# Kernel tuning notes

Hardware: AMD Instinct MI355X
Metric: run time of the kernel (lower is better)

Reference implementation:

```python
import jax, jax.numpy as jnp
import numpy as np

B, BAG, H, C = 512, 32, 1024, 53
EPS = 1e-8  # torch F.cosine_similarity denominator clamp


def setup_inputs() -> dict:
    key = jax.random.key(0)
    ks = jax.random.split(key, 5)
    return {
        "sent_reps": jax.random.normal(ks[0], (B, BAG, H), jnp.float32),
        "aug_sent_reps": jax.random.normal(ks[1], (B, BAG, H), jnp.float32),
        "rel_table": jax.random.normal(ks[2], (C, H), jnp.float32),
        "cls_w": jax.random.normal(ks[3], (C, H), jnp.float32) * 0.02,
        "cls_b": jnp.zeros((C,), jnp.float32),
        "labels": jax.random.randint(ks[4], (B,), 0, C),
        "temperature": jnp.asarray(0.1, jnp.float32),
    }


def _cl(rep, aug, bag_rep, T):
    # rep, aug: (B, bag, H); bag_rep: (B, H)
    nr = jnp.linalg.norm(rep, axis=-1)        # (B, bag)
    na = jnp.linalg.norm(aug, axis=-1)        # (B, bag)
    nb = jnp.linalg.norm(bag_rep, axis=-1)    # (B,)
    pos_sim = jnp.sum(rep * aug, axis=-1) / jnp.maximum(nr * na, EPS)  # (B, bag)
    pos = jnp.exp(pos_sim / T)
    # pair[c, j, b] = cos(rep[b, j], bag_rep[c])  -- matches torch permute/broadcast chain
    dots = jnp.einsum('bjh,ch->cjb', rep, bag_rep)               # (B, bag, B)
    denom = jnp.maximum(nb[:, None, None] * nr.T[None], EPS)      # (B, bag, B)
    pair = dots / denom
    idx = jnp.arange(rep.shape[0])
    axis_sim = pair[idx, :, idx]                                  # (B, bag): cos(rep[b,j], bag_rep[b])
    neg = jnp.exp(pair / T).sum(axis=2) - jnp.exp(axis_sim / T)   # (B, bag)
    return jnp.mean(-jnp.log(pos / (pos + neg)))


def reference(sent_reps, aug_sent_reps, rel_table, cls_w, cls_b, labels, temperature):
    # Selective attention per bag (scope slices are uniform bags of size BAG -> vectorized)
    rel = rel_table[labels]                                        # (B, H)
    scale = jnp.sqrt(jnp.asarray(H, sent_reps.dtype))
    scores = jnp.einsum('bh,bjh->bj', rel, sent_reps) / scale      # (B, bag)
    alphas = jax.nn.softmax(scores, axis=-1)
    bag_reps = jnp.einsum('bj,bjh->bh', alphas, sent_reps)         # (B, H)
    bag_out = bag_reps @ cls_w.T + cls_b                           # (B, C)  (dropout in eval = identity)
    cl_loss = _cl(sent_reps, aug_sent_reps, bag_reps, temperature)
    return bag_out, cl_loss
```

## Files before the change

### kernel.cpp

```cpp
#include <hip/hip_runtime.h>
#include <hip/hip_bf16.h>


typedef __bf16 bf16x8 __attribute__((ext_vector_type(8)));
typedef __bf16 bf16x4 __attribute__((ext_vector_type(4)));
typedef __bf16 bf16x2 __attribute__((ext_vector_type(2)));
typedef float  f32x4  __attribute__((ext_vector_type(4)));

__device__ inline float wsum(float v) {
    #pragma unroll
    for (int off = 32; off > 0; off >>= 1) v += __shfl_xor(v, off, 64);
    return v;
}

__device__ inline void gll16(const void* g, void* l) {
    __builtin_amdgcn_global_load_lds((const __attribute__((address_space(1))) void*)g,
                                     (__attribute__((address_space(3))) void*)l, 16, 0, 0);
}

__device__ inline f32x4 ntld(const float* p) {
    return __builtin_nontemporal_load((const f32x4*)p);
}

__global__ __launch_bounds__(512, 4) void kab(
    const float* __restrict__ sent, const float* __restrict__ aug,
    const float* __restrict__ rel_table, const int* __restrict__ labels,
    __bf16* __restrict__ repb, float* __restrict__ nr, float* __restrict__ pos_sim,
    const float* __restrict__ clsw, __bf16* __restrict__ cwb,
    __bf16* __restrict__ bagb, float* __restrict__ nbsq, float* __restrict__ loss)
{
    __shared__ __align__(16) __bf16 repS[32][1024];
    __shared__ float scoreS[32], alphaS[32], redS[8];
    const int b = blockIdx.x, t = threadIdx.x;
    const int w = t >> 6, lane = t & 63;

    if (b < 128) {
        const int i = b * 512 + t;
        cwb[i] = (i < 53 * 1024) ? (__bf16)clsw[i] : (__bf16)0.0f;
        if (b == 0 && t == 0) *loss = 0.0f;
    }

    const float* relp = rel_table + (size_t)labels[b] * 1024;
    #pragma unroll
    for (int rr = 0; rr < 4; rr++) {
        const int j = w * 4 + rr;
        const size_t rbase = ((size_t)b * 32 + j) * 1024;
        const float* srow = sent + rbase;
        const float* arow = aug + rbase;
        float P = 0.f, R = 0.f, A = 0.f, D = 0.f;
        #pragma unroll
        for (int i = 0; i < 4; i++) {
            const int h = i * 256 + lane * 4;
            f32x4 v  = ntld(srow + h);
            f32x4 a  = ntld(arow + h);
            f32x4 rl = *(const f32x4*)(relp + h);
            P += v.x * rl.x + v.y * rl.y + v.z * rl.z + v.w * rl.w;
            R += v.x * v.x + v.y * v.y + v.z * v.z + v.w * v.w;
            A += a.x * a.x + a.y * a.y + a.z * a.z + a.w * a.w;
            D += v.x * a.x + v.y * a.y + v.z * a.z + v.w * a.w;
            bf16x4 vb = { (__bf16)v.x, (__bf16)v.y, (__bf16)v.z, (__bf16)v.w };
            *(bf16x4*)(&repS[j][h]) = vb;
            *(bf16x4*)(repb + rbase + h) = vb;
        }
        #pragma unroll
        for (int off = 32; off > 0; off >>= 1) {
            P += __shfl_xor(P, off, 64);
            R += __shfl_xor(R, off, 64);
            A += __shfl_xor(A, off, 64);
            D += __shfl_xor(D, off, 64);
        }
        if (lane == 0) {
            scoreS[j] = P * (1.0f / 32.0f);
            float nrv = sqrtf(R), nav = sqrtf(A);
            nr[b * 32 + j] = nrv;
            pos_sim[b * 32 + j] = D / fmaxf(nrv * nav, 1e-8f);
        }
    }
    __syncthreads();

    if (t < 32) {
        float sj = scoreS[t], mx = sj;
        #pragma unroll
        for (int off = 16; off > 0; off >>= 1) mx = fmaxf(mx, __shfl_xor(mx, off, 32));
        float e = __expf(sj - mx), sm = e;
        #pragma unroll
        for (int off = 16; off > 0; off >>= 1) sm += __shfl_xor(sm, off, 32);
        alphaS[t] = e / sm;
    }
    __syncthreads();

    float b0 = 0.f, b1 = 0.f;
    #pragma unroll 8
    for (int j = 0; j < 32; j++) {
        const float al = alphaS[j];
        bf16x2 v = *(const bf16x2*)(&repS[j][t * 2]);
        b0 += al * (float)v.x;
        b1 += al * (float)v.y;
    }
    bf16x2 bb = { (__bf16)b0, (__bf16)b1 };
    *(bf16x2*)(bagb + (size_t)b * 1024 + t * 2) = bb;

    float q = b0 * b0 + b1 * b1;
    q = wsum(q);
    if (lane == 0) redS[w] = q;
    __syncthreads();
    if (t == 0)
        nbsq[b] = redS[0] + redS[1] + redS[2] + redS[3]
                + redS[4] + redS[5] + redS[6] + redS[7];
}

__global__ __launch_bounds__(512, 2) void k4_gemm(
    const __bf16* __restrict__ repb, const __bf16* __restrict__ bagb,
    const float* __restrict__ nr, const float* __restrict__ nbsq,
    const float* __restrict__ temp, float* __restrict__ partial, float* __restrict__ diag,
    const __bf16* __restrict__ cwb, const float* __restrict__ bias, float* __restrict__ out)
{
    __shared__ __align__(16) char smem[98304];
    const int bid = blockIdx.x;
    const int t = threadIdx.x, lane = t & 63, w = t >> 6;
    const int m = lane & 15, quad = lane >> 4;

    if (bid >= 256) {
        __bf16* Al = (__bf16*)smem;
        __bf16* Bl = (__bf16*)(smem + 8192);
        const int r0 = (bid - 256) * 64;
        f32x4 acc[4] = {};
        const int i0 = (t & 255) * 8;
        const int row0 = i0 >> 5, kk0 = i0 & 31;
        const __bf16* gA = bagb + (size_t)(r0 + row0) * 1024 + kk0;
        const __bf16* gB = cwb + (size_t)row0 * 1024 + kk0;
        const bool act = (t < 256);
        for (int k0 = 0; k0 < 1024; k0 += 64) {
            __syncthreads();
            if (act) {
                gll16(gA + k0,      Al + i0);
                gll16(gA + k0 + 32, Al + 2048 + i0);
                gll16(gB + k0,      Bl + i0);
                gll16(gB + k0 + 32, Bl + 2048 + i0);
            }
            __syncthreads();
            if (act) {
                #pragma unroll
                for (int ks = 0; ks < 2; ks++) {
                    bf16x8 a = *(const bf16x8*)(&Al[ks * 2048 + ((t >> 6) * 16 + m) * 32 + quad * 8]);
                    #pragma unroll
                    for (int n = 0; n < 4; n++) {
                        bf16x8 bf = *(const bf16x8*)(&Bl[ks * 2048 + (n * 16 + m) * 32 + quad * 8]);
                        acc[n] = __builtin_amdgcn_mfma_f32_16x16x32_bf16(a, bf, acc[n], 0, 0, 0);
                    }
                }
            }
        }
        if (act) {
            #pragma unroll
            for (int n = 0; n < 4; n++) {
                const int c = n * 16 + m;
                if (c < 53) {
                    #pragma unroll
                    for (int i = 0; i < 4; i++) {
                        const int r = r0 + (t >> 6) * 16 + quad * 4 + i;
                        out[(size_t)r * 53 + c] = acc[n][i] + bias[c];
                    }
                }
            }
        }
        return;
    }

    float* negp4 = (float*)smem;

    const int xcd = bid & 7, slot = bid >> 3;
    const int cb = slot & 3, rb = (slot >> 2) * 8 + xcd;
    const int r0 = rb * 256, c0 = cb * 128;
    const int wr0 = (w & 3) * 64, wc0 = (w >> 2) * 64;

    const int srow = t >> 2;
    const int scol = 8 * ((t & 3) ^ ((t >> 3) & 3));
    const __bf16* gA0 = repb + (size_t)(r0 + srow) * 1024 + scol;
    const __bf16* gA1 = gA0 + (size_t)128 * 1024;
    const __bf16* gB0 = bagb + (size_t)(c0 + srow) * 1024 + scol;
    const int dA0 = t * 8, dA1 = (t + 512) * 8, dB0 = 8192 + t * 8;

    const int rho = (m >> 1) & 3;
    const int offA = ((wr0 + m) * 4 + (quad ^ rho)) * 8;
    const int offB = 8192 + ((wc0 + m) * 4 + (quad ^ rho)) * 8;

    f32x4 acc[4][4] = {};

    #define BUFB(s) ((__bf16*)(smem + (((s) & 3) * 24576)))
    #define STG(s) do { const int kk_ = (s) * 32; __bf16* b_ = BUFB(s);     \
        gll16(gA0 + kk_, b_ + dA0); gll16(gA1 + kk_, b_ + dA1);             \
        gll16(gB0 + kk_, b_ + dB0); } while (0)

    #define CMP(s) do { const __bf16* b_ = BUFB(s); bf16x8 av_[4], bv_[4];  \
        _Pragma("unroll") for (int i_ = 0; i_ < 4; i_++)                    \
            av_[i_] = *(const bf16x8*)(b_ + offA + i_ * 512);               \
        _Pragma("unroll") for (int n_ = 0; n_ < 4; n_++)                    \
            bv_[n_] = *(const bf16x8*)(b_ + offB + n_ * 512);               \
        _Pragma("unroll") for (int i_ = 0; i_ < 4; i_++)                    \
        _Pragma("unroll") for (int n_ = 0; n_ < 4; n_++)                    \
            acc[i_][n_] = __builtin_amdgcn_mfma_f32_16x16x32_bf16(          \
                av_[i_], bv_[n_], acc[i_][n_], 0, 0, 0); } while (0)

    #define FENCE(N) do { __builtin_amdgcn_sched_barrier(0);                \
        asm volatile("s_waitcnt vmcnt(" #N ")" ::: "memory");               \
        __builtin_amdgcn_s_barrier();                                       \
        __builtin_amdgcn_sched_barrier(0); } while (0)

    STG(0); STG(1); STG(2);
    FENCE(6);
    #pragma unroll 1
    for (int s = 0; s < 29; ++s) {
        STG(s + 3);
        CMP(s);
        FENCE(6);
    }
    CMP(29); FENCE(3);
    CMP(30); FENCE(0);
    CMP(31);

    const float invT = 1.0f / *temp;
    float nrv[16];
    #pragma unroll
    for (int i = 0; i < 4; i++)
        #pragma unroll
        for (int g = 0; g < 4; g++)
            nrv[i * 4 + g] = nr[r0 + wr0 + i * 16 + quad * 4 + g];

    float* myneg = negp4 + (size_t)(w & 3) * 32 * 128;
    #pragma unroll
    for (int n = 0; n < 4; n++) {
        const int c_local = wc0 + n * 16 + m;
        const int cg = c0 + c_local;
        const float nbv = sqrtf(nbsq[cg]);
        #pragma unroll
        for (int i = 0; i < 2; i++) {
            #pragma unroll
            for (int g = 0; g < 4; g++) {
                const int jj = i * 16 + quad * 4 + g;
                const int rg0 = r0 + wr0 + i * 16 + quad * 4 + g;
                const int rg2 = rg0 + 32;
                float e0 = __expf(acc[i][n][g]     / fmaxf(nbv * nrv[i * 4 + g],       1e-8f) * invT);
                float e2 = __expf(acc[i + 2][n][g] / fmaxf(nbv * nrv[(i + 2) * 4 + g], 1e-8f) * invT);
                myneg[jj * 128 + c_local] = e0 + e2;
                if ((rg0 >> 5) == cg) diag[(size_t)cg * 32 + jj] = e0;
                if ((rg2 >> 5) == cg) diag[(size_t)cg * 32 + jj] = e2;
            }
        }
    }
    __syncthreads();

    float* pout = partial + (size_t)rb * 32 * 512 + c0;
    {
        const int jj = t >> 4, c8 = (t & 15) * 8;
        f32x4 v0 = {}, v1 = {};
        #pragma unroll
        for (int p = 0; p < 4; p++) {
            const float* src = negp4 + (size_t)p * 32 * 128 + jj * 128 + c8;
            v0 += *(const f32x4*)(src);
            v1 += *(const f32x4*)(src + 4);
        }
        *(f32x4*)(pout + (size_t)jj * 512 + c8)     = v0;
        *(f32x4*)(pout + (size_t)jj * 512 + c8 + 4) = v1;
    }
    #undef BUFB
    #undef STG
    #undef CMP
    #undef FENCE
}

__global__ __launch_bounds__(256) void k5_neg(
    const float* __restrict__ partial, const float* __restrict__ diag,
    const float* __restrict__ pos_sim, const float* __restrict__ temp,
    float* __restrict__ loss)
{
    const int ct = blockIdx.x & 7, j = blockIdx.x >> 3;
    const int t = threadIdx.x, lane = t & 63, w = t >> 6;
    const int bsub = t >> 4;
    const int cidx = t & 15;
    f32x4 acc = {};
    #pragma unroll
    for (int r = 0; r < 4; r++) {
        const int rb = bsub * 4 + r;
        f32x4 v = *(const f32x4*)(partial + ((size_t)rb * 32 + j) * 512 + ct * 64 + cidx * 4);
        acc += v;
    }
    #pragma unroll
    for (int k = 0; k < 4; k++) {
        acc[k] += __shfl_xor(acc[k], 16, 64);
        acc[k] += __shfl_xor(acc[k], 32, 64);
    }
    __shared__ float red[4][64];
    if (lane < 16) {
        #pragma unroll
        for (int k = 0; k < 4; k++) red[w][lane * 4 + k] = acc[k];
    }
    __syncthreads();

    if (t < 64) {
        const int c = ct * 64 + t;
        float S = red[0][t] + red[1][t] + red[2][t] + red[3][t];
        S -= diag[(size_t)c * 32 + j];
        const float invT = 1.0f / *temp;
        const float lp = pos_sim[(c << 5) + j] * invT;
        float term = logf(__expf(lp) + S) - lp;
        term = wsum(term);
        if (t == 0) atomicAdd(loss, term * (1.0f / 16384.0f));
    }
}

extern "C" void kernel_launch(void* const* d_in, const int* in_sizes, int n_in,
                              void* d_out, int out_size, void* d_ws, size_t ws_size,
                              hipStream_t stream)
{
    const float* sent = (const float*)d_in[0];
    const float* aug  = (const float*)d_in[1];
    const float* rel  = (const float*)d_in[2];
    const float* clsw = (const float*)d_in[3];
    const float* clsb = (const float*)d_in[4];
    const int*   lab  = (const int*)d_in[5];
    const float* temp = (const float*)d_in[6];
    float* out = (float*)d_out;

    char* ws = (char*)d_ws;
    __bf16* bagb    = (__bf16*)(ws);
    float*  nbsq    = (float*)(ws + (1u << 20));
    float*  nr      = (float*)(ws + (1u << 20) + 64 * 1024);
    float*  pos     = (float*)(ws + (1u << 20) + 128 * 1024);
    __bf16* cwb     = (__bf16*)(ws + (1u << 20) + 192 * 1024);
    float*  diag    = (float*)(ws + (2u << 20) + 64 * 1024);
    __bf16* repb    = (__bf16*)(ws + (4u << 20));
    float*  partial = (float*)(ws + (36u << 20));

    float* loss = out + 27136;

    kab    <<<512, 512, 0, stream>>>(sent, aug, rel, lab, repb, nr, pos,
                                     clsw, cwb, bagb, nbsq, loss);
    k4_gemm<<<264, 512, 0, stream>>>(repb, bagb, nr, nbsq, temp, partial, diag,
                                     cwb, clsb, out);
    k5_neg <<<256, 256, 0, stream>>>(partial, diag, pos, temp, loss);
}
```

Baseline: 197.6 us.

## Halve GEMM row tile to 128 with 256-thread blocks and triple-buffered LDS

The contrastive GEMM block shrinks from 256x128 tiles with 8 waves to 128x128 tiles with 4 waves. The grid roughly doubles to 520 blocks, and the LDS pipeline drops from 4 stages to 3 at 48KB. The classifier GEMM blocks move to the front of the grid, and the partial-sum reduction grows to 16 row-blocks. The aim is better occupancy and CU load balance across 256 CUs, in exchange for more partial traffic and less A/B reuse per block.

```diff
diff --git a/kernel.cpp b/kernel.cpp
--- a/kernel.cpp
+++ b/kernel.cpp
@@ -109,88 +109,84 @@
                 + redS[4] + redS[5] + redS[6] + redS[7];
 }
 
-__global__ __launch_bounds__(512, 2) void k4_gemm(
+__global__ __launch_bounds__(256, 3) void k4_gemm(
     const __bf16* __restrict__ repb, const __bf16* __restrict__ bagb,
     const float* __restrict__ nr, const float* __restrict__ nbsq,
     const float* __restrict__ temp, float* __restrict__ partial, float* __restrict__ diag,
     const __bf16* __restrict__ cwb, const float* __restrict__ bias, float* __restrict__ out)
 {
-    __shared__ __align__(16) char smem[98304];
+    __shared__ __align__(16) char smem[49152];
     const int bid = blockIdx.x;
     const int t = threadIdx.x, lane = t & 63, w = t >> 6;
     const int m = lane & 15, quad = lane >> 4;
 
-    if (bid >= 256) {
+    if (bid < 8) {
         __bf16* Al = (__bf16*)smem;
         __bf16* Bl = (__bf16*)(smem + 8192);
-        const int r0 = (bid - 256) * 64;
+        const int r0 = bid * 64;
         f32x4 acc[4] = {};
-        const int i0 = (t & 255) * 8;
+        const int i0 = t * 8;
         const int row0 = i0 >> 5, kk0 = i0 & 31;
         const __bf16* gA = bagb + (size_t)(r0 + row0) * 1024 + kk0;
         const __bf16* gB = cwb + (size_t)row0 * 1024 + kk0;
-        const bool act = (t < 256);
         for (int k0 = 0; k0 < 1024; k0 += 64) {
             __syncthreads();
-            if (act) {
-                gll16(gA + k0,      Al + i0);
-                gll16(gA + k0 + 32, Al + 2048 + i0);
-                gll16(gB + k0,      Bl + i0);
-                gll16(gB + k0 + 32, Bl + 2048 + i0);
-            }
+            gll16(gA + k0,      Al + i0);
+            gll16(gA + k0 + 32, Al + 2048 + i0);
+            gll16(gB + k0,      Bl + i0);
+            gll16(gB + k0 + 32, Bl + 2048 + i0);
             __syncthreads();
-            if (act) {
+            #pragma unroll
+            for (int ks = 0; ks < 2; ks++) {
+                bf16x8 a = *(const bf16x8*)(&Al[ks * 2048 + (w * 16 + m) * 32 + quad * 8]);
                 #pragma unroll
-                for (int ks = 0; ks < 2; ks++) {
-                    bf16x8 a = *(const bf16x8*)(&Al[ks * 2048 + ((t >> 6) * 16 + m) * 32 + quad * 8]);
-                    #pragma unroll
-                    for (int n = 0; n < 4; n++) {
-                        bf16x8 bf = *(const bf16x8*)(&Bl[ks * 2048 + (n * 16 + m) * 32 + quad * 8]);
-                        acc[n] = __builtin_amdgcn_mfma_f32_16x16x32_bf16(a, bf, acc[n], 0, 0, 0);
-                    }
+                for (int n = 0; n < 4; n++) {
+                    bf16x8 bf = *(const bf16x8*)(&Bl[ks * 2048 + (n * 16 + m) * 32 + quad * 8]);
+                    acc[n] = __builtin_amdgcn_mfma_f32_16x16x32_bf16(a, bf, acc[n], 0, 0, 0);
                 }
             }
         }
-        if (act) {
-            #pragma unroll
-            for (int n = 0; n < 4; n++) {
-                const int c = n * 16 + m;
-                if (c < 53) {
-                    #pragma unroll
-                    for (int i = 0; i < 4; i++) {
-                        const int r = r0 + (t >> 6) * 16 + quad * 4 + i;
-                        out[(size_t)r * 53 + c] = acc[n][i] + bias[c];
-                    }
+        #pragma unroll
+        for (int n = 0; n < 4; n++) {
+            const int c = n * 16 + m;
+            if (c < 53) {
+                #pragma unroll
+                for (int i = 0; i < 4; i++) {
+                    const int r = r0 + w * 16 + quad * 4 + i;
+                    out[(size_t)r * 53 + c] = acc[n][i] + bias[c];
                 }
             }
         }
         return;
     }
 
-    float* negp4 = (float*)smem;
-
-    const int xcd = bid & 7, slot = bid >> 3;
+    float* negp2 = (float*)smem;
+
+    const int gbid = bid - 8;
+    const int xcd = gbid & 7, slot = gbid >> 3;
     const int cb = slot & 3, rb = (slot >> 2) * 8 + xcd;
-    const int r0 = rb * 256, c0 = cb * 128;
-    const int wr0 = (w & 3) * 64, wc0 = (w >> 2) * 64;
+    const int r0 = rb * 128, c0 = cb * 128;
+    const int wr0 = (w & 1) * 64, wc0 = (w >> 1) * 64;
 
     const int srow = t >> 2;
-    const int scol = 8 * ((t & 3) ^ ((t >> 3) & 3));
+    const int scol = 8 * ((t & 3) ^ ((srow >> 1) & 3));
     const __bf16* gA0 = repb + (size_t)(r0 + srow) * 1024 + scol;
-    const __bf16* gA1 = gA0 + (size_t)128 * 1024;
+    const __bf16* gA1 = gA0 + (size_t)64 * 1024;
     const __bf16* gB0 = bagb + (size_t)(c0 + srow) * 1024 + scol;
-    const int dA0 = t * 8, dA1 = (t + 512) * 8, dB0 = 8192 + t * 8;
+    const __bf16* gB1 = gB0 + (size_t)64 * 1024;
+    const int dA0 = t * 8, dA1 = (t + 256) * 8;
+    const int dB0 = 4096 + t * 8, dB1 = 4096 + (t + 256) * 8;
 
     const int rho = (m >> 1) & 3;
     const int offA = ((wr0 + m) * 4 + (quad ^ rho)) * 8;
-    const int offB = 8192 + ((wc0 + m) * 4 + (quad ^ rho)) * 8;
+    const int offB = 4096 + ((wc0 + m) * 4 + (quad ^ rho)) * 8;
 
     f32x4 acc[4][4] = {};
 
-    #define BUFB(s) ((__bf16*)(smem + (((s) & 3) * 24576)))
+    #define BUFB(s) ((__bf16*)(smem + (((s) % 3) * 16384)))
     #define STG(s) do { const int kk_ = (s) * 32; __bf16* b_ = BUFB(s);     \
         gll16(gA0 + kk_, b_ + dA0); gll16(gA1 + kk_, b_ + dA1);             \
-        gll16(gB0 + kk_, b_ + dB0); } while (0)
+        gll16(gB0 + kk_, b_ + dB0); gll16(gB1 + kk_, b_ + dB1); } while (0)
 
     #define CMP(s) do { const __bf16* b_ = BUFB(s); bf16x8 av_[4], bv_[4];  \
         _Pragma("unroll") for (int i_ = 0; i_ < 4; i_++)                    \
@@ -207,17 +203,17 @@
         __builtin_amdgcn_s_barrier();                                       \
         __builtin_amdgcn_sched_barrier(0); } while (0)
 
-    STG(0); STG(1); STG(2);
-    FENCE(6);
+    STG(0); STG(1);
+    FENCE(4);
     #pragma unroll 1
-    for (int s = 0; s < 29; ++s) {
-        STG(s + 3);
+    for (int s = 0; s < 30; ++s) {
+        STG(s + 2);
         CMP(s);
-        FENCE(6);
-    }
-    CMP(29); FENCE(3);
+        FENCE(4);
+    }
     CMP(30); FENCE(0);
     CMP(31);
+    __syncthreads();
 
     const float invT = 1.0f / *temp;
     float nrv[16];
@@ -227,7 +223,7 @@
         for (int g = 0; g < 4; g++)
             nrv[i * 4 + g] = nr[r0 + wr0 + i * 16 + quad * 4 + g];
 
-    float* myneg = negp4 + (size_t)(w & 3) * 32 * 128;
+    float* myneg = negp2 + (size_t)(w & 1) * 32 * 128;
     #pragma unroll
     for (int n = 0; n < 4; n++) {
         const int c_local = wc0 + n * 16 + m;
@@ -252,16 +248,13 @@
 
     float* pout = partial + (size_t)rb * 32 * 512 + c0;
     {
-        const int jj = t >> 4, c8 = (t & 15) * 8;
-        f32x4 v0 = {}, v1 = {};
-        #pragma unroll
-        for (int p = 0; p < 4; p++) {
-            const float* src = negp4 + (size_t)p * 32 * 128 + jj * 128 + c8;
-            v0 += *(const f32x4*)(src);
-            v1 += *(const f32x4*)(src + 4);
-        }
-        *(f32x4*)(pout + (size_t)jj * 512 + c8)     = v0;
-        *(f32x4*)(pout + (size_t)jj * 512 + c8 + 4) = v1;
+        const int jj = t >> 3, c16 = (t & 7) * 16;
+        #pragma unroll
+        for (int v = 0; v < 4; v++) {
+            f32x4 a = *(const f32x4*)(negp2 + jj * 128 + c16 + v * 4);
+            f32x4 bq = *(const f32x4*)(negp2 + 32 * 128 + jj * 128 + c16 + v * 4);
+            *(f32x4*)(pout + (size_t)jj * 512 + c16 + v * 4) = a + bq;
+        }
     }
     #undef BUFB
     #undef STG
@@ -279,9 +272,9 @@
     const int bsub = t >> 4;
     const int cidx = t & 15;
     f32x4 acc = {};
-    #pragma unroll
-    for (int r = 0; r < 4; r++) {
-        const int rb = bsub * 4 + r;
+    #pragma unroll 4
+    for (int r = 0; r < 8; r++) {
+        const int rb = bsub * 8 + r;
         f32x4 v = *(const f32x4*)(partial + ((size_t)rb * 32 + j) * 512 + ct * 64 + cidx * 4);
         acc += v;
     }
@@ -336,7 +329,7 @@
 
     kab    <<<512, 512, 0, stream>>>(sent, aug, rel, lab, repb, nr, pos,
                                      clsw, cwb, bagb, nbsq, loss);
-    k4_gemm<<<264, 512, 0, stream>>>(repb, bagb, nr, nbsq, temp, partial, diag,
+    k4_gemm<<<520, 256, 0, stream>>>(repb, bagb, nr, nbsq, temp, partial, diag,
                                      cwb, clsb, out);
     k5_neg <<<256, 256, 0, stream>>>(partial, diag, pos, temp, loss);
 }
```

After: 189.8 us. 1.04x faster.
